# Optimization experiments

Measured on AMD Instinct MI355X. Metric: run time of the kernel, lower is better.

Reference implementation:

```python
import jax, jax.numpy as jnp
import numpy as np

N = 10000       # nodes
E = 320000      # edges (avg degree 32)
F_IN = 128      # node_in_fts
F_OUT = 128     # node_out_fts
H = 4           # num_heads_node
E_IN = 64       # edge_in_fts
HOPS = 3        # nr_of_hops
SLOPE = 0.2     # LeakyReLU negative slope (GAT default)


def setup_inputs() -> dict:
    key = jax.random.key(0)
    ks = jax.random.split(key, 10)
    s = 0.05
    return {
        "node_fts": jax.random.normal(ks[0], (N, F_IN), dtype=jnp.float32),
        "edge_fts": jax.random.normal(ks[1], (E, E_IN), dtype=jnp.float32),
        "edges": jax.random.randint(ks[2], (2, E), 0, N),
        # per-hop GATConv params (all hops share dims, stacked on axis 0)
        "Ws": jax.random.normal(ks[3], (HOPS, F_IN, H * F_OUT), dtype=jnp.float32) * s,
        "Wes": jax.random.normal(ks[4], (HOPS, E_IN, H * F_OUT), dtype=jnp.float32) * s,
        "a_src": jax.random.normal(ks[5], (HOPS, H, F_OUT), dtype=jnp.float32) * s,
        "a_dst": jax.random.normal(ks[6], (HOPS, H, F_OUT), dtype=jnp.float32) * s,
        "a_edge": jax.random.normal(ks[7], (HOPS, H, F_OUT), dtype=jnp.float32) * s,
        # gated residual params
        "W_prior": jax.random.normal(ks[8], (F_OUT, F_OUT), dtype=jnp.float32) * s,
        "W_curr": jax.random.normal(ks[9], (F_OUT, F_OUT), dtype=jnp.float32) * s,
    }


def _gat_conv(x, edge_fts, src, dst, W, We, asrc, adst, aedge):
    # dense projections: [N,H,F_OUT] and [E,H,F_OUT]
    h = (x @ W).reshape(-1, H, F_OUT)
    he = (edge_fts @ We).reshape(-1, H, F_OUT)
    h_src = h[src]                                   # [E,H,F_OUT] gather
    # per-edge attention logits [E,H]
    alpha = (h_src * asrc).sum(-1) + (h[dst] * adst).sum(-1) + (he * aedge).sum(-1)
    alpha = jax.nn.leaky_relu(alpha, SLOPE)
    # segment softmax over incoming edges of each destination node
    amax = jnp.full((N, H), -jnp.inf, dtype=alpha.dtype).at[dst].max(alpha)
    w = jnp.exp(alpha - amax[dst])                   # [E,H]
    denom = jax.ops.segment_sum(w, dst, num_segments=N) + 1e-16  # [N,H]
    msg = w[:, :, None] * h_src                      # [E,H,F_OUT]
    out = jax.ops.segment_sum(msg, dst, num_segments=N) / denom[:, :, None]
    return out.mean(axis=1)                          # mean head aggregation -> [N,F_OUT]


def reference(node_fts, edge_fts, edges, Ws, Wes, a_src, a_dst, a_edge, W_prior, W_curr):
    src, dst = edges[0], edges[1]
    x = node_fts
    prior = None
    for i in range(HOPS):
        curr = _gat_conv(x, edge_fts, src, dst, Ws[i], Wes[i], a_src[i], a_dst[i], a_edge[i])
        if prior is None:
            x = curr
        else:
            gate = jax.nn.sigmoid(prior @ W_prior + curr @ W_curr)
            x = gate * curr + (1.0 - gate) * prior
        prior = x
    return x
```

## Files before the change

kernel.cpp:

```cpp
#include <hip/hip_runtime.h>
#include <hip/hip_fp16.h>

#define N_NODES 10000
#define E_EDGES 320000
#define NH 4
#define HOPS 3
#define WMAX 128

typedef _Float16 f16x8 __attribute__((ext_vector_type(8)));
typedef _Float16 f16x4 __attribute__((ext_vector_type(4)));
typedef float    f32x4 __attribute__((ext_vector_type(4)));

__global__ void k_count(const int* __restrict__ dst, int* __restrict__ counts){
  int e = blockIdx.x*256 + threadIdx.x;
  if(e < E_EDGES) atomicAdd(&counts[dst[e]], 1);
}

__global__ __launch_bounds__(1024) void k_scan(const int* __restrict__ counts,
                                               int* __restrict__ row_ptr, int* __restrict__ fillp){
  __shared__ int sm[1024];
  int t = threadIdx.x;
  const int CH = 10;
  int base = t*CH;
  int loc[CH]; int sum = 0;
  #pragma unroll
  for(int i=0;i<CH;i++){
    int v = (base+i < N_NODES) ? counts[base+i] : 0;
    loc[i] = sum; sum += v;
  }
  sm[t] = sum; __syncthreads();
  for(int off=1; off<1024; off<<=1){
    int add = (t>=off) ? sm[t-off] : 0;
    __syncthreads();
    sm[t] += add;
    __syncthreads();
  }
  int excl = (t>0) ? sm[t-1] : 0;
  #pragma unroll
  for(int i=0;i<CH;i++){
    int n = base+i;
    if(n < N_NODES){
      int e = excl + loc[i];
      row_ptr[n] = e;
      fillp[n]   = e;
    }
  }
  if(t==1023) row_ptr[N_NODES] = sm[1023];
}

__global__ void k_fill(const int* __restrict__ src, const int* __restrict__ dst,
                       int* __restrict__ fillp, int* __restrict__ csr_eid, int* __restrict__ sorted_src){
  int e = blockIdx.x*256 + threadIdx.x;
  if(e < E_EDGES){
    int d = dst[e];
    int pos = atomicAdd(&fillp[d], 1);
    csr_eid[pos] = e;
    sorted_src[pos] = src[e];
  }
}

__global__ __launch_bounds__(256) void k_setup(const float* __restrict__ node_fts, _Float16* __restrict__ xh,
                       const float* __restrict__ Ws, _Float16* __restrict__ WsT,
                       const float* __restrict__ Wes, const float* __restrict__ a_edge,
                       float* __restrict__ b_edge){
  __shared__ float lds[32][65];
  int b = blockIdx.x, t = threadIdx.x;
  if(b < 1250){
    int i = b*256 + t;
    float4 v = *(const float4*)(node_fts + (size_t)i*4);
    f16x4 h = { (_Float16)v.x, (_Float16)v.y, (_Float16)v.z, (_Float16)v.w };
    *(f16x4*)(xh + (size_t)i*4) = h;
  } else if(b < 1346){
    int b2 = b - 1250;
    int hop = b2>>5, rem = b2&31, kt = rem>>3, ct = rem&7;
    int k0 = kt*32, c0 = ct*64;
    const float* wsrc = Ws + (size_t)hop*65536;
    #pragma unroll
    for(int i=0;i<8;i++){
      int u = t + i*256;
      int kk = u>>6, cc = u&63;
      lds[kk][cc] = wsrc[(size_t)(k0+kk)*512 + c0 + cc];
    }
    __syncthreads();
    _Float16* wdst = WsT + (size_t)hop*512*128;
    #pragma unroll
    for(int i=0;i<2;i++){
      int u = t + i*256;
      int c = u>>3, kq = (u&7)*4;
      f16x4 h = { (_Float16)lds[kq][c], (_Float16)lds[kq+1][c],
                  (_Float16)lds[kq+2][c], (_Float16)lds[kq+3][c] };
      *(f16x4*)(wdst + (size_t)(c0+c)*128 + k0 + kq) = h;
    }
  } else {
    int idx = (b-1346)*256 + t;
    if(idx < HOPS*64*NH){
      int hop = idx/(64*NH); int c = (idx/NH)%64; int h = idx%NH;
      const float* we = Wes + (size_t)hop*64*512 + (size_t)c*512 + h*128;
      const float* ae = a_edge + (size_t)hop*NH*128 + h*128;
      float s = 0.f;
      for(int f=0; f<128; f++) s += we[f] * ae[f];
      b_edge[idx] = s;
    }
  }
}

__global__ __launch_bounds__(256) void k_alpha_mfma(const float* __restrict__ edge_fts,
                        const int* __restrict__ csr_eid, const float* __restrict__ b_edge,
                        float* __restrict__ ae_sorted){
  __shared__ float tile[64][20];
  int w = threadIdx.x>>6, l = threadIdx.x&63;
  int col = l&15, kgrp = l>>4;
  f16x8 bf0, bf1;
  #pragma unroll
  for(int j=0;j<8;j++){
    int k0 = 0*32 + kgrp*8 + j;
    int k1 = 1*32 + kgrp*8 + j;
    float v0 = 0.f, v1 = 0.f;
    if(col < 12){
      int hop = col>>2, h = col&3;
      v0 = b_edge[hop*256 + k0*4 + h];
      v1 = b_edge[hop*256 + k1*4 + h];
    }
    bf0[j] = (_Float16)v0;
    bf1[j] = (_Float16)v1;
  }
  int pos0 = blockIdx.x*64 + w*16;
  int erow = csr_eid[pos0 + (l&15)];
  const float* ef = edge_fts + (size_t)erow*64 + kgrp*8;
  f32x4 acc = {0.f,0.f,0.f,0.f};
  {
    float4 x0 = *(const float4*)(ef);
    float4 x1 = *(const float4*)(ef + 4);
    f16x8 a = { (_Float16)x0.x,(_Float16)x0.y,(_Float16)x0.z,(_Float16)x0.w,
                (_Float16)x1.x,(_Float16)x1.y,(_Float16)x1.z,(_Float16)x1.w };
    acc = __builtin_amdgcn_mfma_f32_16x16x32_f16(a, bf0, acc, 0, 0, 0);
  }
  {
    float4 x0 = *(const float4*)(ef + 32);
    float4 x1 = *(const float4*)(ef + 36);
    f16x8 a = { (_Float16)x0.x,(_Float16)x0.y,(_Float16)x0.z,(_Float16)x0.w,
                (_Float16)x1.x,(_Float16)x1.y,(_Float16)x1.z,(_Float16)x1.w };
    acc = __builtin_amdgcn_mfma_f32_16x16x32_f16(a, bf1, acc, 0, 0, 0);
  }
  int crow = (l>>4)*4;
  #pragma unroll
  for(int r=0;r<4;r++) tile[w*16 + crow + r][col] = acc[r];
  __syncthreads();
  int u = threadIdx.x;
  int edge = u>>2, q = u&3;
  if(q < 3){
    *(float4*)(ae_sorted + (size_t)q*E_EDGES*4 + ((size_t)(blockIdx.x*64 + edge))*4)
      = *(const float4*)&tile[edge][q*4];
  }
}

__global__ __launch_bounds__(256) void k_projm(const _Float16* __restrict__ xh,
                       const _Float16* __restrict__ Wt, __half* __restrict__ h_all){
  __shared__ __align__(16) __half tile[64][72];
  int w = threadIdx.x>>6, l = threadIdx.x&63;
  int rowb = blockIdx.x*64;
  int row0 = rowb + w*16;
  int col0 = blockIdx.y*64;
  int ar = l&15, ac = (l>>4)*8;
  f32x4 acc0 = {0.f,0.f,0.f,0.f}, acc1 = acc0, acc2 = acc0, acc3 = acc0;
  #pragma unroll
  for(int kk=0; kk<4; kk++){
    f16x8 a  = *(const f16x8*)(xh + (size_t)(row0+ar)*128 + kk*32 + ac);
    f16x8 b0 = *(const f16x8*)(Wt + (size_t)(col0 +  0 + ar)*128 + kk*32 + ac);
    f16x8 b1 = *(const f16x8*)(Wt + (size_t)(col0 + 16 + ar)*128 + kk*32 + ac);
    f16x8 b2 = *(const f16x8*)(Wt + (size_t)(col0 + 32 + ar)*128 + kk*32 + ac);
    f16x8 b3 = *(const f16x8*)(Wt + (size_t)(col0 + 48 + ar)*128 + kk*32 + ac);
    acc0 = __builtin_amdgcn_mfma_f32_16x16x32_f16(a, b0, acc0, 0, 0, 0);
    acc1 = __builtin_amdgcn_mfma_f32_16x16x32_f16(a, b1, acc1, 0, 0, 0);
    acc2 = __builtin_amdgcn_mfma_f32_16x16x32_f16(a, b2, acc2, 0, 0, 0);
    acc3 = __builtin_amdgcn_mfma_f32_16x16x32_f16(a, b3, acc3, 0, 0, 0);
  }
  int crow = (l>>4)*4, ccol = l&15;
  #pragma unroll
  for(int r=0; r<4; r++){
    int tr = w*16 + crow + r;
    tile[tr][ccol     ] = __float2half(acc0[r]);
    tile[tr][ccol + 16] = __float2half(acc1[r]);
    tile[tr][ccol + 32] = __float2half(acc2[r]);
    tile[tr][ccol + 48] = __float2half(acc3[r]);
  }
  __syncthreads();
  #pragma unroll
  for(int i=0;i<2;i++){
    int u = threadIdx.x + i*256;
    int row = u>>3, cq = (u&7)*8;
    int grow = rowb + row;
    if(grow < N_NODES)
      *(float4*)(h_all + (size_t)grow*512 + col0 + cq) = *(const float4*)&tile[row][cq];
  }
}

__global__ __launch_bounds__(256) void k_s(const __half* __restrict__ h_all, const float* __restrict__ asrc,
                    const float* __restrict__ adst, float* __restrict__ s_src, float* __restrict__ s_dst){
  int nw = blockIdx.x*4 + (threadIdx.x>>6);
  int l = threadIdx.x&63;
  if(nw >= N_NODES) return;
  int h = l>>4, f8 = (l&15)*8;
  const __half* hp = h_all + (size_t)nw*512 + (h<<7) + f8;
  float4 raw = *(const float4*)hp;
  const __half2* hh = (const __half2*)&raw;
  float2 c0 = __half22float2(hh[0]);
  float2 c1 = __half22float2(hh[1]);
  float2 c2 = __half22float2(hh[2]);
  float2 c3 = __half22float2(hh[3]);
  float4 a0 = *(const float4*)(asrc + (h<<7) + f8);
  float4 a1 = *(const float4*)(asrc + (h<<7) + f8 + 4);
  float4 d0 = *(const float4*)(adst + (h<<7) + f8);
  float4 d1 = *(const float4*)(adst + (h<<7) + f8 + 4);
  float ps = c0.x*a0.x + c0.y*a0.y + c1.x*a0.z + c1.y*a0.w
           + c2.x*a1.x + c2.y*a1.y + c3.x*a1.z + c3.y*a1.w;
  float pd = c0.x*d0.x + c0.y*d0.y + c1.x*d0.z + c1.y*d0.w
           + c2.x*d1.x + c2.y*d1.y + c3.x*d1.z + c3.y*d1.w;
  #pragma unroll
  for(int off=1; off<16; off<<=1){ ps += __shfl_xor(ps,off); pd += __shfl_xor(pd,off); }
  if((l&15)==0){ s_src[nw*4+h] = ps; s_dst[nw*4+h] = pd; }
}

__global__ __launch_bounds__(256) void k_softagg(
    const float* __restrict__ ae, const float* __restrict__ s_src,
    const float* __restrict__ s_dst, const int* __restrict__ sorted_src,
    const int* __restrict__ row_ptr, const __half* __restrict__ h_all,
    float* __restrict__ ew_fb, float* __restrict__ xout, _Float16* __restrict__ xh)
{
  __shared__ float ws4[4][WMAX*4];
  __shared__ int   ssm4[4][WMAX];
  int wv = threadIdx.x>>6, l = threadIdx.x&63;
  int n = blockIdx.x*4 + wv;
  if(n >= N_NODES) return;
  int start = row_ptr[n], end = row_ptr[n+1];
  int deg = end - start;
  bool fits = (deg <= WMAX);
  float* ws = ws4[wv];
  int*   ssm = ssm4[wv];

  float4 sd = *(const float4*)(s_dst + (size_t)n*4);
  float m0=-1e30f, m1=-1e30f, m2=-1e30f, m3=-1e30f;
  float aR[2][4];

  if(fits){
    #pragma unroll
    for(int k=0;k<2;k++){
      int idx = l + k*64;
      if(idx < deg){
        int pos = start + idx;
        int s = sorted_src[pos];
        float4 ss = *(const float4*)(s_src + (size_t)s*4);
        float4 av = *(const float4*)(ae + (size_t)pos*4);
        float a0 = ss.x+sd.x+av.x; a0=(a0>0.f)?a0:0.2f*a0;
        float a1 = ss.y+sd.y+av.y; a1=(a1>0.f)?a1:0.2f*a1;
        float a2 = ss.z+sd.z+av.z; a2=(a2>0.f)?a2:0.2f*a2;
        float a3 = ss.w+sd.w+av.w; a3=(a3>0.f)?a3:0.2f*a3;
        aR[k][0]=a0; aR[k][1]=a1; aR[k][2]=a2; aR[k][3]=a3;
        ssm[idx] = s;
        m0=fmaxf(m0,a0); m1=fmaxf(m1,a1); m2=fmaxf(m2,a2); m3=fmaxf(m3,a3);
      }
    }
  } else {
    for(int pos=start+l; pos<end; pos+=64){
      int s = sorted_src[pos];
      float4 ss = *(const float4*)(s_src + (size_t)s*4);
      float4 av = *(const float4*)(ae + (size_t)pos*4);
      float a0 = ss.x+sd.x+av.x; a0=(a0>0.f)?a0:0.2f*a0;
      float a1 = ss.y+sd.y+av.y; a1=(a1>0.f)?a1:0.2f*a1;
      float a2 = ss.z+sd.z+av.z; a2=(a2>0.f)?a2:0.2f*a2;
      float a3 = ss.w+sd.w+av.w; a3=(a3>0.f)?a3:0.2f*a3;
      *(float4*)(ew_fb + (size_t)pos*4) = make_float4(a0,a1,a2,a3);
      m0=fmaxf(m0,a0); m1=fmaxf(m1,a1); m2=fmaxf(m2,a2); m3=fmaxf(m3,a3);
    }
  }
  #pragma unroll
  for(int off=32; off; off>>=1){
    m0=fmaxf(m0,__shfl_xor(m0,off)); m1=fmaxf(m1,__shfl_xor(m1,off));
    m2=fmaxf(m2,__shfl_xor(m2,off)); m3=fmaxf(m3,__shfl_xor(m3,off));
  }

  float s0=0.f,s1=0.f,s2=0.f,s3=0.f;
  if(fits){
    #pragma unroll
    for(int k=0;k<2;k++){
      int idx = l + k*64;
      if(idx < deg){
        float w0=__expf(aR[k][0]-m0), w1=__expf(aR[k][1]-m1);
        float w2=__expf(aR[k][2]-m2), w3=__expf(aR[k][3]-m3);
        int sl = idx*4;
        ws[sl]=w0; ws[sl+1]=w1; ws[sl+2]=w2; ws[sl+3]=w3;
        s0+=w0; s1+=w1; s2+=w2; s3+=w3;
      }
    }
  } else {
    for(int pos=start+l; pos<end; pos+=64){
      float4 a = *(const float4*)(ew_fb + (size_t)pos*4);
      float w0=__expf(a.x-m0), w1=__expf(a.y-m1), w2=__expf(a.z-m2), w3=__expf(a.w-m3);
      *(float4*)(ew_fb + (size_t)pos*4) = make_float4(w0,w1,w2,w3);
      s0+=w0; s1+=w1; s2+=w2; s3+=w3;
    }
  }
  #pragma unroll
  for(int off=32; off; off>>=1){
    s0+=__shfl_xor(s0,off); s1+=__shfl_xor(s1,off);
    s2+=__shfl_xor(s2,off); s3+=__shfl_xor(s3,off);
  }

  int h = l>>4, f8 = (l&15)*8;
  float dh = (h==0)?s0:((h==1)?s1:((h==2)?s2:s3));
  float inv = 1.f/(dh + 1e-16f);
  float ac0[8]={0,0,0,0,0,0,0,0}, ac1[8]={0,0,0,0,0,0,0,0};
  float ac2[8]={0,0,0,0,0,0,0,0}, ac3[8]={0,0,0,0,0,0,0,0};
  int hoff = (h<<7) + f8;
  int sl = 0;
  if(fits){
    for(; sl+4 <= deg; sl+=4){
      int sA = ssm[sl], sB = ssm[sl+1], sC = ssm[sl+2], sD = ssm[sl+3];
      float wA = ws[sl*4+h], wB = ws[(sl+1)*4+h], wC = ws[(sl+2)*4+h], wD = ws[(sl+3)*4+h];
      float4 rA = *(const float4*)(h_all + (size_t)sA*512 + hoff);
      float4 rB = *(const float4*)(h_all + (size_t)sB*512 + hoff);
      float4 rC = *(const float4*)(h_all + (size_t)sC*512 + hoff);
      float4 rD = *(const float4*)(h_all + (size_t)sD*512 + hoff);
      const __half2* hA = (const __half2*)&rA;
      const __half2* hB = (const __half2*)&rB;
      const __half2* hC = (const __half2*)&rC;
      const __half2* hD = (const __half2*)&rD;
      #pragma unroll
      for(int j=0;j<4;j++){
        float2 vA = __half22float2(hA[j]);
        float2 vB = __half22float2(hB[j]);
        float2 vC = __half22float2(hC[j]);
        float2 vD = __half22float2(hD[j]);
        ac0[2*j]+=wA*vA.x; ac0[2*j+1]+=wA*vA.y;
        ac1[2*j]+=wB*vB.x; ac1[2*j+1]+=wB*vB.y;
        ac2[2*j]+=wC*vC.x; ac2[2*j+1]+=wC*vC.y;
        ac3[2*j]+=wD*vD.x; ac3[2*j+1]+=wD*vD.y;
      }
    }
    for(; sl < deg; sl++){
      int s = ssm[sl]; float w = ws[sl*4+h];
      float4 r = *(const float4*)(h_all + (size_t)s*512 + hoff);
      const __half2* hh = (const __half2*)&r;
      #pragma unroll
      for(int j=0;j<4;j++){
        float2 v = __half22float2(hh[j]);
        ac0[2*j]+=w*v.x; ac0[2*j+1]+=w*v.y;
      }
    }
  } else {
    for(; sl < deg; sl++){
      int s = sorted_src[start+sl]; float w = ew_fb[(size_t)(start+sl)*4+h];
      float4 r = *(const float4*)(h_all + (size_t)s*512 + hoff);
      const __half2* hh = (const __half2*)&r;
      #pragma unroll
      for(int j=0;j<4;j++){
        float2 v = __half22float2(hh[j]);
        ac0[2*j]+=w*v.x; ac0[2*j+1]+=w*v.y;
      }
    }
  }
  float acc[8];
  #pragma unroll
  for(int i=0;i<8;i++){
    acc[i] = (ac0[i]+ac1[i]) + (ac2[i]+ac3[i]);
    acc[i] *= inv;
    acc[i] += __shfl_xor(acc[i], 16);
    acc[i] += __shfl_xor(acc[i], 32);
    acc[i] *= 0.25f;
  }
  if(l < 16){
    int f0 = l*8;
    *(float4*)(xout + (size_t)n*128 + f0)     = make_float4(acc[0],acc[1],acc[2],acc[3]);
    *(float4*)(xout + (size_t)n*128 + f0 + 4) = make_float4(acc[4],acc[5],acc[6],acc[7]);
    if(xh){
      f16x8 hv = { (_Float16)acc[0],(_Float16)acc[1],(_Float16)acc[2],(_Float16)acc[3],
                   (_Float16)acc[4],(_Float16)acc[5],(_Float16)acc[6],(_Float16)acc[7] };
      *(f16x8*)(xh + (size_t)n*128 + f0) = hv;
    }
  }
}

__global__ __launch_bounds__(256) void k_gate2(const float* __restrict__ prior, const float* __restrict__ curr,
                       const float* __restrict__ Wp, const float* __restrict__ Wc,
                       float* __restrict__ xnew, _Float16* __restrict__ xh){
  __shared__ float pr[32][132];
  __shared__ float cu[32][132];
  int t = threadIdx.x;
  int n0 = blockIdx.x*32;
  int c0 = blockIdx.y*64;
  #pragma unroll
  for(int i=0;i<4;i++){
    int u = t + i*256;
    int row = u>>5, c4 = (u&31)<<2;
    float4 v = make_float4(0.f,0.f,0.f,0.f), w = v;
    if(n0+row < N_NODES){
      v = *(const float4*)(prior + (size_t)(n0+row)*128 + c4);
      w = *(const float4*)(curr  + (size_t)(n0+row)*128 + c4);
    }
    *(float4*)&pr[row][c4] = v;
    *(float4*)&cu[row][c4] = w;
  }
  __syncthreads();
  int tc = t&15, tr = t>>4;
  int r0 = tr*2, cc = c0 + tc*4;
  float accp[2][4] = {{0.f,0.f,0.f,0.f},{0.f,0.f,0.f,0.f}};
  float accc[2][4] = {{0.f,0.f,0.f,0.f},{0.f,0.f,0.f,0.f}};
  #pragma unroll 4
  for(int k=0;k<128;k++){
    float4 wp = *(const float4*)(Wp + (size_t)k*128 + cc);
    float4 wc = *(const float4*)(Wc + (size_t)k*128 + cc);
    #pragma unroll
    for(int i=0;i<2;i++){
      float ap = pr[r0+i][k], ac = cu[r0+i][k];
      accp[i][0]+=ap*wp.x; accp[i][1]+=ap*wp.y; accp[i][2]+=ap*wp.z; accp[i][3]+=ap*wp.w;
      accc[i][0]+=ac*wc.x; accc[i][1]+=ac*wc.y; accc[i][2]+=ac*wc.z; accc[i][3]+=ac*wc.w;
    }
  }
  #pragma unroll
  for(int i=0;i<2;i++){
    int row = n0 + r0 + i;
    if(row < N_NODES){
      float oj[4];
      #pragma unroll
      for(int j=0;j<4;j++){
        float z = accp[i][j]+accc[i][j];
        float g = 1.f/(1.f+__expf(-z));
        oj[j] = g*cu[r0+i][cc + j] + (1.f-g)*pr[r0+i][cc + j];
      }
      *(float4*)(xnew + (size_t)row*128 + cc) = make_float4(oj[0],oj[1],oj[2],oj[3]);
      if(xh){
        f16x4 hv = { (_Float16)oj[0], (_Float16)oj[1], (_Float16)oj[2], (_Float16)oj[3] };
        *(f16x4*)(xh + (size_t)row*128 + cc) = hv;
      }
    }
  }
}

extern "C" void kernel_launch(void* const* d_in, const int* in_sizes, int n_in,
                              void* d_out, int out_size, void* d_ws, size_t ws_size,
                              hipStream_t stream){
  (void)in_sizes; (void)n_in; (void)out_size; (void)ws_size;
  const float* node_fts = (const float*)d_in[0];
  const float* edge_fts = (const float*)d_in[1];
  const int*   edges    = (const int*)d_in[2];
  const float* Ws       = (const float*)d_in[3];
  const float* Wes      = (const float*)d_in[4];
  const float* a_src    = (const float*)d_in[5];
  const float* a_dst    = (const float*)d_in[6];
  const float* a_edge   = (const float*)d_in[7];
  const float* W_prior  = (const float*)d_in[8];
  const float* W_curr   = (const float*)d_in[9];

  char* ws = (char*)d_ws;
  size_t off = 0;
  auto alloc = [&](size_t bytes)->void*{
    void* p = ws + off;
    off += (bytes + 255) & ~(size_t)255;
    return p;
  };
  int*       counts     = (int*)      alloc((size_t)N_NODES*4);
  int*       row_ptr    = (int*)      alloc((size_t)(N_NODES+1)*4);
  int*       fillp      = (int*)      alloc((size_t)N_NODES*4);
  int*       csr_eid    = (int*)      alloc((size_t)E_EDGES*4);
  int*       sorted_src = (int*)      alloc((size_t)E_EDGES*4);
  float*     b_edge     = (float*)    alloc((size_t)HOPS*64*NH*4);
  float*     ae_sorted  = (float*)    alloc((size_t)HOPS*E_EDGES*NH*4);
  __half*    h_all      = (__half*)   alloc((size_t)N_NODES*512*2);
  float*     s_src      = (float*)    alloc((size_t)N_NODES*NH*4);
  float*     s_dst      = (float*)    alloc((size_t)N_NODES*NH*4);
  float*     ew_fb      = (float*)    alloc((size_t)E_EDGES*NH*4);
  float*     xbuf       = (float*)    alloc((size_t)N_NODES*128*4);
  float*     curbuf     = (float*)    alloc((size_t)N_NODES*128*4);
  _Float16*  xh         = (_Float16*) alloc((size_t)10112*128*2);
  _Float16*  WsT        = (_Float16*) alloc((size_t)HOPS*512*128*2);

  const int* src = edges;
  const int* dst = edges + E_EDGES;

  (void)hipMemsetAsync(counts, 0, (size_t)N_NODES*4, stream);
  k_count<<<(E_EDGES+255)/256, 256, 0, stream>>>(dst, counts);
  k_scan<<<1, 1024, 0, stream>>>(counts, row_ptr, fillp);
  k_fill<<<(E_EDGES+255)/256, 256, 0, stream>>>(src, dst, fillp, csr_eid, sorted_src);
  k_setup<<<1349, 256, 0, stream>>>(node_fts, xh, Ws, WsT, Wes, a_edge, b_edge);
  k_alpha_mfma<<<5000, 256, 0, stream>>>(edge_fts, csr_eid, b_edge, ae_sorted);

  for(int hop=0; hop<HOPS; hop++){
    k_projm<<<dim3(157, 8), 256, 0, stream>>>(xh, WsT + (size_t)hop*512*128, h_all);
    k_s<<<2500, 256, 0, stream>>>(h_all, a_src + (size_t)hop*512, a_dst + (size_t)hop*512, s_src, s_dst);
    float* xout = (hop==0) ? xbuf : curbuf;
    k_softagg<<<2500, 256, 0, stream>>>(ae_sorted + (size_t)hop*E_EDGES*4, s_src, s_dst,
                                        sorted_src, row_ptr, h_all, ew_fb, xout,
                                        (hop==0) ? xh : (_Float16*)nullptr);
    if(hop > 0){
      float* xnew = (hop == HOPS-1) ? (float*)d_out : xbuf;
      k_gate2<<<dim3(313, 2), 256, 0, stream>>>(xbuf, curbuf, W_prior, W_curr, xnew,
                                                (hop < HOPS-1) ? xh : (_Float16*)nullptr);
    }
  }
}
```

Before: 315.3 us.

## Fuse attention-score dot products into projection GEMM and widen aggregation gather batch

The projection kernel now computes one full head (128 columns) per block, and in its epilogue dots the fp32 accumulators with a_src/a_dst, writing s_src/s_dst directly. This removes the separate k_s kernel, its launch, and its re-read of h_all. Each block now holds twice as many accumulators, which raises register pressure and halves the grid in y. The softmax-aggregation loop also issues eight neighbor gathers at once before accumulating, so more memory loads are in flight.

```diff
diff --git a/kernel.cpp b/kernel.cpp
--- a/kernel.cpp
+++ b/kernel.cpp
@@ -155,70 +155,69 @@
 }
 
 __global__ __launch_bounds__(256) void k_projm(const _Float16* __restrict__ xh,
-                       const _Float16* __restrict__ Wt, __half* __restrict__ h_all){
-  __shared__ __align__(16) __half tile[64][72];
+                       const _Float16* __restrict__ Wt, __half* __restrict__ h_all,
+                       const float* __restrict__ asrc, const float* __restrict__ adst,
+                       float* __restrict__ s_src, float* __restrict__ s_dst){
+  __shared__ __align__(16) __half tile[64][136];
   int w = threadIdx.x>>6, l = threadIdx.x&63;
   int rowb = blockIdx.x*64;
   int row0 = rowb + w*16;
-  int col0 = blockIdx.y*64;
+  int head = blockIdx.y;
+  int col0 = head*128;
   int ar = l&15, ac = (l>>4)*8;
-  f32x4 acc0 = {0.f,0.f,0.f,0.f}, acc1 = acc0, acc2 = acc0, acc3 = acc0;
+  f32x4 acc[8];
+  #pragma unroll
+  for(int q=0;q<8;q++) acc[q] = (f32x4){0.f,0.f,0.f,0.f};
   #pragma unroll
   for(int kk=0; kk<4; kk++){
-    f16x8 a  = *(const f16x8*)(xh + (size_t)(row0+ar)*128 + kk*32 + ac);
-    f16x8 b0 = *(const f16x8*)(Wt + (size_t)(col0 +  0 + ar)*128 + kk*32 + ac);
-    f16x8 b1 = *(const f16x8*)(Wt + (size_t)(col0 + 16 + ar)*128 + kk*32 + ac);
-    f16x8 b2 = *(const f16x8*)(Wt + (size_t)(col0 + 32 + ar)*128 + kk*32 + ac);
-    f16x8 b3 = *(const f16x8*)(Wt + (size_t)(col0 + 48 + ar)*128 + kk*32 + ac);
-    acc0 = __builtin_amdgcn_mfma_f32_16x16x32_f16(a, b0, acc0, 0, 0, 0);
-    acc1 = __builtin_amdgcn_mfma_f32_16x16x32_f16(a, b1, acc1, 0, 0, 0);
-    acc2 = __builtin_amdgcn_mfma_f32_16x16x32_f16(a, b2, acc2, 0, 0, 0);
-    acc3 = __builtin_amdgcn_mfma_f32_16x16x32_f16(a, b3, acc3, 0, 0, 0);
+    f16x8 a = *(const f16x8*)(xh + (size_t)(row0+ar)*128 + kk*32 + ac);
+    #pragma unroll
+    for(int q=0;q<8;q++){
+      f16x8 b = *(const f16x8*)(Wt + (size_t)(col0 + q*16 + ar)*128 + kk*32 + ac);
+      acc[q] = __builtin_amdgcn_mfma_f32_16x16x32_f16(a, b, acc[q], 0, 0, 0);
+    }
   }
   int crow = (l>>4)*4, ccol = l&15;
-  #pragma unroll
-  for(int r=0; r<4; r++){
-    int tr = w*16 + crow + r;
-    tile[tr][ccol     ] = __float2half(acc0[r]);
-    tile[tr][ccol + 16] = __float2half(acc1[r]);
-    tile[tr][ccol + 32] = __float2half(acc2[r]);
-    tile[tr][ccol + 48] = __float2half(acc3[r]);
+  {
+    float ps[4] = {0.f,0.f,0.f,0.f}, pd[4] = {0.f,0.f,0.f,0.f};
+    #pragma unroll
+    for(int q=0;q<8;q++){
+      float as_ = asrc[col0 + q*16 + ccol];
+      float ad_ = adst[col0 + q*16 + ccol];
+      #pragma unroll
+      for(int r=0;r<4;r++){ ps[r] += acc[q][r]*as_; pd[r] += acc[q][r]*ad_; }
+    }
+    #pragma unroll
+    for(int m=1;m<16;m<<=1){
+      #pragma unroll
+      for(int r=0;r<4;r++){ ps[r] += __shfl_xor(ps[r], m); pd[r] += __shfl_xor(pd[r], m); }
+    }
+    if(ccol == 0){
+      #pragma unroll
+      for(int r=0;r<4;r++){
+        int row = row0 + crow + r;
+        if(row < N_NODES){
+          s_src[(size_t)row*4 + head] = ps[r];
+          s_dst[(size_t)row*4 + head] = pd[r];
+        }
+      }
+    }
+  }
+  #pragma unroll
+  for(int q=0;q<8;q++){
+    #pragma unroll
+    for(int r=0;r<4;r++)
+      tile[w*16 + crow + r][q*16 + ccol] = __float2half(acc[q][r]);
   }
   __syncthreads();
   #pragma unroll
-  for(int i=0;i<2;i++){
+  for(int i=0;i<4;i++){
     int u = threadIdx.x + i*256;
-    int row = u>>3, cq = (u&7)*8;
+    int row = u>>4, cq = (u&15)*8;
     int grow = rowb + row;
     if(grow < N_NODES)
       *(float4*)(h_all + (size_t)grow*512 + col0 + cq) = *(const float4*)&tile[row][cq];
   }
-}
-
-__global__ __launch_bounds__(256) void k_s(const __half* __restrict__ h_all, const float* __restrict__ asrc,
-                    const float* __restrict__ adst, float* __restrict__ s_src, float* __restrict__ s_dst){
-  int nw = blockIdx.x*4 + (threadIdx.x>>6);
-  int l = threadIdx.x&63;
-  if(nw >= N_NODES) return;
-  int h = l>>4, f8 = (l&15)*8;
-  const __half* hp = h_all + (size_t)nw*512 + (h<<7) + f8;
-  float4 raw = *(const float4*)hp;
-  const __half2* hh = (const __half2*)&raw;
-  float2 c0 = __half22float2(hh[0]);
-  float2 c1 = __half22float2(hh[1]);
-  float2 c2 = __half22float2(hh[2]);
-  float2 c3 = __half22float2(hh[3]);
-  float4 a0 = *(const float4*)(asrc + (h<<7) + f8);
-  float4 a1 = *(const float4*)(asrc + (h<<7) + f8 + 4);
-  float4 d0 = *(const float4*)(adst + (h<<7) + f8);
-  float4 d1 = *(const float4*)(adst + (h<<7) + f8 + 4);
-  float ps = c0.x*a0.x + c0.y*a0.y + c1.x*a0.z + c1.y*a0.w
-           + c2.x*a1.x + c2.y*a1.y + c3.x*a1.z + c3.y*a1.w;
-  float pd = c0.x*d0.x + c0.y*d0.y + c1.x*d0.z + c1.y*d0.w
-           + c2.x*d1.x + c2.y*d1.y + c3.x*d1.z + c3.y*d1.w;
-  #pragma unroll
-  for(int off=1; off<16; off<<=1){ ps += __shfl_xor(ps,off); pd += __shfl_xor(pd,off); }
-  if((l&15)==0){ s_src[nw*4+h] = ps; s_dst[nw*4+h] = pd; }
 }
 
 __global__ __launch_bounds__(256) void k_softagg(
@@ -309,32 +308,46 @@
   int h = l>>4, f8 = (l&15)*8;
   float dh = (h==0)?s0:((h==1)?s1:((h==2)?s2:s3));
   float inv = 1.f/(dh + 1e-16f);
-  float ac0[8]={0,0,0,0,0,0,0,0}, ac1[8]={0,0,0,0,0,0,0,0};
-  float ac2[8]={0,0,0,0,0,0,0,0}, ac3[8]={0,0,0,0,0,0,0,0};
+  float ac[4][8] = {{0,0,0,0,0,0,0,0},{0,0,0,0,0,0,0,0},{0,0,0,0,0,0,0,0},{0,0,0,0,0,0,0,0}};
   int hoff = (h<<7) + f8;
   int sl = 0;
   if(fits){
+    for(; sl+8 <= deg; sl+=8){
+      float wg[8]; float4 rr[8];
+      #pragma unroll
+      for(int j=0;j<8;j++){
+        int s = ssm[sl+j];
+        wg[j] = ws[(sl+j)*4+h];
+        rr[j] = *(const float4*)(h_all + (size_t)s*512 + hoff);
+      }
+      #pragma unroll
+      for(int j=0;j<8;j++){
+        const __half2* hh = (const __half2*)&rr[j];
+        #pragma unroll
+        for(int q=0;q<4;q++){
+          float2 v = __half22float2(hh[q]);
+          ac[j&3][2*q]   += wg[j]*v.x;
+          ac[j&3][2*q+1] += wg[j]*v.y;
+        }
+      }
+    }
     for(; sl+4 <= deg; sl+=4){
-      int sA = ssm[sl], sB = ssm[sl+1], sC = ssm[sl+2], sD = ssm[sl+3];
-      float wA = ws[sl*4+h], wB = ws[(sl+1)*4+h], wC = ws[(sl+2)*4+h], wD = ws[(sl+3)*4+h];
-      float4 rA = *(const float4*)(h_all + (size_t)sA*512 + hoff);
-      float4 rB = *(const float4*)(h_all + (size_t)sB*512 + hoff);
-      float4 rC = *(const float4*)(h_all + (size_t)sC*512 + hoff);
-      float4 rD = *(const float4*)(h_all + (size_t)sD*512 + hoff);
-      const __half2* hA = (const __half2*)&rA;
-      const __half2* hB = (const __half2*)&rB;
-      const __half2* hC = (const __half2*)&rC;
-      const __half2* hD = (const __half2*)&rD;
+      float wg[4]; float4 rr[4];
       #pragma unroll
       for(int j=0;j<4;j++){
-        float2 vA = __half22float2(hA[j]);
-        float2 vB = __half22float2(hB[j]);
-        float2 vC = __half22float2(hC[j]);
-        float2 vD = __half22float2(hD[j]);
-        ac0[2*j]+=wA*vA.x; ac0[2*j+1]+=wA*vA.y;
-        ac1[2*j]+=wB*vB.x; ac1[2*j+1]+=wB*vB.y;
-        ac2[2*j]+=wC*vC.x; ac2[2*j+1]+=wC*vC.y;
-        ac3[2*j]+=wD*vD.x; ac3[2*j+1]+=wD*vD.y;
+        int s = ssm[sl+j];
+        wg[j] = ws[(sl+j)*4+h];
+        rr[j] = *(const float4*)(h_all + (size_t)s*512 + hoff);
+      }
+      #pragma unroll
+      for(int j=0;j<4;j++){
+        const __half2* hh = (const __half2*)&rr[j];
+        #pragma unroll
+        for(int q=0;q<4;q++){
+          float2 v = __half22float2(hh[q]);
+          ac[j][2*q]   += wg[j]*v.x;
+          ac[j][2*q+1] += wg[j]*v.y;
+        }
       }
     }
     for(; sl < deg; sl++){
@@ -342,9 +355,10 @@
       float4 r = *(const float4*)(h_all + (size_t)s*512 + hoff);
       const __half2* hh = (const __half2*)&r;
       #pragma unroll
-      for(int j=0;j<4;j++){
-        float2 v = __half22float2(hh[j]);
-        ac0[2*j]+=w*v.x; ac0[2*j+1]+=w*v.y;
+      for(int q=0;q<4;q++){
+        float2 v = __half22float2(hh[q]);
+        ac[0][2*q]   += w*v.x;
+        ac[0][2*q+1] += w*v.y;
       }
     }
   } else {
@@ -353,16 +367,17 @@
       float4 r = *(const float4*)(h_all + (size_t)s*512 + hoff);
       const __half2* hh = (const __half2*)&r;
       #pragma unroll
-      for(int j=0;j<4;j++){
-        float2 v = __half22float2(hh[j]);
-        ac0[2*j]+=w*v.x; ac0[2*j+1]+=w*v.y;
+      for(int q=0;q<4;q++){
+        float2 v = __half22float2(hh[q]);
+        ac[0][2*q]   += w*v.x;
+        ac[0][2*q+1] += w*v.y;
       }
     }
   }
   float acc[8];
   #pragma unroll
   for(int i=0;i<8;i++){
-    acc[i] = (ac0[i]+ac1[i]) + (ac2[i]+ac3[i]);
+    acc[i] = (ac[0][i]+ac[1][i]) + (ac[2][i]+ac[3][i]);
     acc[i] *= inv;
     acc[i] += __shfl_xor(acc[i], 16);
     acc[i] += __shfl_xor(acc[i], 32);
@@ -485,8 +500,9 @@
   k_alpha_mfma<<<5000, 256, 0, stream>>>(edge_fts, csr_eid, b_edge, ae_sorted);
 
   for(int hop=0; hop<HOPS; hop++){
-    k_projm<<<dim3(157, 8), 256, 0, stream>>>(xh, WsT + (size_t)hop*512*128, h_all);
-    k_s<<<2500, 256, 0, stream>>>(h_all, a_src + (size_t)hop*512, a_dst + (size_t)hop*512, s_src, s_dst);
+    k_projm<<<dim3(157, 4), 256, 0, stream>>>(xh, WsT + (size_t)hop*512*128, h_all,
+                                              a_src + (size_t)hop*512, a_dst + (size_t)hop*512,
+                                              s_src, s_dst);
     float* xout = (hop==0) ? xbuf : curbuf;
     k_softagg<<<2500, 256, 0, stream>>>(ae_sorted + (size_t)hop*E_EDGES*4, s_src, s_dst,
                                         sorted_src, row_ptr, h_all, ew_fb, xout,
```

Result: slower. 333.2 us (+5.7%).
